# Optimization experiments

Hardware: AMD Instinct MI355X
Metric: run time of the kernel (lower is better)

## Reference

```python
import jax, jax.numpy as jnp
import numpy as np
import math

B, D, NH, NS, NT = 16, 256, 512, 8, 32
NV = NS * NT          # 256 prediction variables
L, H, A = 4, 8, 64    # attention layers, heads, head dim
HA = H * A            # 512
M = 512               # mlp_dim
R = 128               # resolution
EPS = 1e-5


def setup_inputs() -> dict:
    key = jax.random.key(0)
    ks = jax.random.split(key, 32)
    s = 0.02
    inp = {
        'hist_encoded': jax.random.normal(ks[0], (B, NH, D), jnp.float32),
        'hist_true_u': jax.random.uniform(ks[1], (B, NH), jnp.float32),
        'pred_encoded': jax.random.normal(ks[2], (B, NV, D), jnp.float32),
        'pred_true_u': jax.random.uniform(ks[3], (B, NV), jnp.float32),
        # dimension shifting layer
        'ds_w': jax.random.normal(ks[4], (D, HA), jnp.float32) * s,
        'ds_b': jnp.zeros((HA,), jnp.float32),
        # per-layer, per-head key/value creators: Linear(D+1 -> A)
        'key_w': jax.random.normal(ks[5], (L, H, D + 1, A), jnp.float32) * s,
        'key_b': jnp.zeros((L, H, A), jnp.float32),
        'val_w': jax.random.normal(ks[6], (L, H, D + 1, A), jnp.float32) * s,
        'val_b': jnp.zeros((L, H, A), jnp.float32),
        # layer norms
        'ln1_g': jnp.ones((L, HA), jnp.float32),
        'ln1_b': jnp.zeros((L, HA), jnp.float32),
        'ln2_g': jnp.ones((L, HA), jnp.float32),
        'ln2_b': jnp.zeros((L, HA), jnp.float32),
        # feed-forward (mlp_layers=2): HA->M, M->M, M->HA
        'ff_w1': jax.random.normal(ks[7], (L, HA, M), jnp.float32) * s,
        'ff_b1': jnp.zeros((L, M), jnp.float32),
        'ff_w2': jax.random.normal(ks[8], (L, M, M), jnp.float32) * s,
        'ff_b2': jnp.zeros((L, M), jnp.float32),
        'ff_w3': jax.random.normal(ks[9], (L, M, HA), jnp.float32) * s,
        'ff_b3': jnp.zeros((L, HA), jnp.float32),
        # dist extractor
        'de_w': jax.random.normal(ks[10], (HA, R), jnp.float32) * s,
        'de_b': jnp.zeros((R,), jnp.float32),
        'num_series': NS,
        'num_timesteps': NT,
    }
    return inp


def _ln(x, g, b):
    m = x.mean(-1, keepdims=True)
    v = ((x - m) ** 2).mean(-1, keepdims=True)
    return g * (x - m) / jnp.sqrt(v + EPS) + b


def _forward(hist_encoded, hist_true_u, pred_encoded, pred_true_u,
             ds_w, ds_b, key_w, key_b, val_w, val_b,
             ln1_g, ln1_b, ln2_g, ln2_b,
             ff_w1, ff_b1, ff_w2, ff_b2, ff_w3, ff_b3,
             de_w, de_b):
    Bm, NVm, Dm = pred_encoded.shape
    NHm = hist_encoded.shape[1]
    Lm, Hm, _, Am = key_w.shape
    W = NHm + NVm
    # identity permutation in the source loss() -> no-op
    att = pred_encoded @ ds_w + ds_b  # [B, NV, HA]
    # key/value inputs: [hist||u ; pred||u] -> [B, W, D+1]
    ki = jnp.concatenate([
        jnp.concatenate([hist_encoded, hist_true_u[:, :, None]], axis=2),
        jnp.concatenate([pred_encoded, pred_true_u[:, :, None]], axis=2)], axis=1)
    keys = jnp.einsum('bwd,lhda->lbhwa', ki, key_w) + key_b[:, None, :, None, :]
    vals = jnp.einsum('bwd,lhda->lbhwa', ki, val_w) + val_b[:, None, :, None, :]
    # flipped-triangular mask: position w is masked iff w >= NH + v
    mask = jnp.arange(W)[None, :] >= (NHm + jnp.arange(NVm)[:, None])  # [NV, W]
    scale = Am ** (-0.5)
    for l in range(Lm):
        avh = att.reshape(Bm, NVm, Hm, Am)
        prod = jnp.einsum('bvhi,bhwi->bhvw', avh, keys[l])  # [B,H,NV,W]
        prod = jnp.where(mask, -jnp.inf, prod) * scale
        w = jax.nn.softmax(prod, axis=-1)
        a = jnp.einsum('bhvw,bhwj->bvhj', w, vals[l]).reshape(Bm, NVm, Hm * Am)
        att = _ln(att + a, ln1_g[l], ln1_b[l])
        ff = jnp.maximum(att @ ff_w1[l] + ff_b1[l], 0.0)
        ff = jnp.maximum(ff @ ff_w2[l] + ff_b2[l], 0.0)
        ff = ff @ ff_w3[l] + ff_b3[l]
        att = _ln(att + ff, ln2_g[l], ln2_b[l])
    res = de_w.shape[-1]
    target = jnp.clip(jnp.floor(pred_true_u[:, 1:] * res).astype(jnp.int32), 0, res - 1)
    logits = (att @ de_w + de_b)[:, 1:, :]
    lp = math.log(res) + jax.nn.log_softmax(logits, axis=2)
    lp = jnp.take_along_axis(lp, target[:, :, None], axis=2)[:, :, 0]
    return -lp.sum(axis=1)  # [B]


def reference(hist_encoded, hist_true_u, pred_encoded, pred_true_u,
              ds_w, ds_b, key_w, key_b, val_w, val_b,
              ln1_g, ln1_b, ln2_g, ln2_b,
              ff_w1, ff_b1, ff_w2, ff_b2, ff_w3, ff_b3,
              de_w, de_b, num_series, num_timesteps):
    assert pred_encoded.shape[1] == num_series * num_timesteps
    return _forward(hist_encoded, hist_true_u, pred_encoded, pred_true_u,
                    ds_w, ds_b, key_w, key_b, val_w, val_b,
                    ln1_g, ln1_b, ln2_g, ln2_b,
                    ff_w1, ff_b1, ff_w2, ff_b2, ff_w3, ff_b3,
                    de_w, de_b)
```

## Files before the change

### kernel.cpp

```cpp
#include <hip/hip_runtime.h>

constexpr int kB = 16, kD = 256, kNH = 512, kNV = 256, kW = 768;
constexpr int kL = 4, kH = 8, kA = 64, kHA = 512, kM = 512, kR = 128;
constexpr int kKP = 288;
constexpr int kRows = kB * kNV;

typedef __bf16 bf16x8 __attribute__((ext_vector_type(8)));
typedef __bf16 bf16x4 __attribute__((ext_vector_type(4)));
typedef __bf16 bf16x2 __attribute__((ext_vector_type(2)));
typedef float f32x4 __attribute__((ext_vector_type(4)));

__device__ inline void load_lds16(const __bf16* g, __bf16* l) {
  __builtin_amdgcn_global_load_lds(
      (const __attribute__((address_space(1))) void*)g,
      (__attribute__((address_space(3))) void*)l, 16, 0, 0);
}

constexpr int kPrepBlocks = 10769;

__global__ void prep_kernel(const float* __restrict__ hist,
                            const float* __restrict__ hist_u,
                            const float* __restrict__ pred,
                            const float* __restrict__ pred_u,
                            const float* __restrict__ kw,
                            const float* __restrict__ vw,
                            const float* __restrict__ w1,
                            const float* __restrict__ w2,
                            const float* __restrict__ w3,
                            const float* __restrict__ ds_w,
                            const float* __restrict__ de_w,
                            const float* __restrict__ key_b,
                            const float* __restrict__ val_b,
                            __bf16* __restrict__ ki,
                            __bf16* __restrict__ kvwt,
                            __bf16* __restrict__ ffwt,
                            __bf16* __restrict__ ds_wt,
                            __bf16* __restrict__ de_wt,
                            float* __restrict__ kvb,
                            float* __restrict__ outz) {
  __shared__ float ld[2080];
  const int bid = blockIdx.x;
  const int t = threadIdx.x;
  if (bid < 6912) {
    int i = bid * 512 + t * 2;
    __bf16 v2[2];
#pragma unroll
    for (int e = 0; e < 2; ++e) {
      int ii = i + e;
      int d = ii % kKP;
      int bw = ii / kKP;
      int w = bw % kW;
      int b = bw / kW;
      float v = 0.f;
      if (d < 257) {
        if (w < kNH)
          v = (d < kD) ? hist[((size_t)b * kNH + w) * kD + d]
                       : hist_u[b * kNH + w];
        else {
          int p = w - kNH;
          v = (d < kD) ? pred[((size_t)b * kNV + p) * kD + d]
                       : pred_u[b * kNV + p];
        }
      }
      v2[e] = (__bf16)v;
    }
    *(bf16x2*)&ki[i] = bf16x2{v2[0], v2[1]};
  } else if (bid < 7488) {
    int bb = bid - 6912;
    bool isv = bb >= 288;
    int rem = isv ? bb - 288 : bb;
    int pair = rem / 9;
    int dt = rem - pair * 9;
    int d0 = dt * 32;
    const float* src = (isv ? vw : kw) + (size_t)pair * 257 * 64;
    int a = t & 63, dg = t >> 6;
#pragma unroll
    for (int ii = 0; ii < 8; ++ii) {
      int d = d0 + dg * 8 + ii;
      ld[(dg * 8 + ii) * 65 + a] = (d < 257) ? src[(size_t)d * 64 + a] : 0.f;
    }
    __syncthreads();
    int r = t >> 2, seg = t & 3;
    bf16x8 v;
#pragma unroll
    for (int j = 0; j < 8; ++j) v[j] = (__bf16)ld[(seg * 8 + j) * 65 + r];
    *(bf16x8*)&kvwt[((size_t)(isv ? 2048 : 0) + pair * 64 + r) * 288 + d0 +
                    seg * 8] = v;
  } else if (bid < 10560) {
    int cc = bid - 7488;
    int mat = cc >> 8;
    int tile = cc & 255;
    int n0 = (tile & 15) * 32, k0 = (tile >> 4) * 32;
    int l = mat / 3, which = mat - l * 3;
    const float* src = (which == 0 ? w1 : which == 1 ? w2 : w3) +
                       (size_t)l * 262144;
    int col = t & 31, kr = t >> 5;
#pragma unroll
    for (int p = 0; p < 4; ++p)
      ld[(kr + p * 8) * 33 + col] = src[(size_t)(k0 + kr + p * 8) * 512 + n0 + col];
    __syncthreads();
    int nr = t >> 3, seg = t & 7;
    bf16x4 v;
#pragma unroll
    for (int j = 0; j < 4; ++j) v[j] = (__bf16)ld[(seg * 4 + j) * 33 + nr];
    *(bf16x4*)&ffwt[(size_t)mat * 262144 + (n0 + nr) * 512 + k0 + seg * 4] = v;
  } else if (bid < 10688) {
    int cc = bid - 10560;
    int n0 = (cc & 15) * 32, k0 = (cc >> 4) * 32;
    int col = t & 31, kr = t >> 5;
#pragma unroll
    for (int p = 0; p < 4; ++p)
      ld[(kr + p * 8) * 33 + col] = ds_w[(size_t)(k0 + kr + p * 8) * 512 + n0 + col];
    __syncthreads();
    int nr = t >> 3, seg = t & 7;
    bf16x4 v;
#pragma unroll
    for (int j = 0; j < 4; ++j) v[j] = (__bf16)ld[(seg * 4 + j) * 33 + nr];
    *(bf16x4*)&ds_wt[(n0 + nr) * 256 + k0 + seg * 4] = v;
  } else if (bid < 10752) {
    int cc = bid - 10688;
    int n0 = (cc & 3) * 32, k0 = (cc >> 2) * 32;
    int col = t & 31, kr = t >> 5;
#pragma unroll
    for (int p = 0; p < 4; ++p)
      ld[(kr + p * 8) * 33 + col] = de_w[(size_t)(k0 + kr + p * 8) * 128 + n0 + col];
    __syncthreads();
    int nr = t >> 3, seg = t & 7;
    bf16x4 v;
#pragma unroll
    for (int j = 0; j < 4; ++j) v[j] = (__bf16)ld[(seg * 4 + j) * 33 + nr];
    *(bf16x4*)&de_wt[(n0 + nr) * 512 + k0 + seg * 4] = v;
  } else {
    int j = (bid - 10752) * 256 + t;
    if (j < 4096) {
      bool isv = j >= 2048;
      int cc = isv ? j - 2048 : j;
      int l = cc >> 9, rest = cc & 511;
      kvb[j] = isv ? val_b[l * 512 + rest] : key_b[l * 512 + rest];
    } else if (j < 4112) {
      outz[j - 4096] = 0.f;
    }
  }
}

template <int BN, int OMODE, bool RELU, bool KIMAP, bool BIASROW, int DEPTH>
__device__ __forceinline__ void gemm_core(
    int bxv, int byv, const __bf16* __restrict__ A,
    const __bf16* __restrict__ Bt, const float* __restrict__ bias,
    void* __restrict__ Cout, __bf16* __restrict__ Cout2, int K, int lda,
    int ldc, __bf16* Sm) {
  constexpr int JN = BN / 32;
  constexpr int BROWS = BN / 4;
  constexpr int SSTEP = (128 + BN) * 32;
  constexpr int LPS = (BN == 128) ? 4 : 3;
  constexpr int AH = DEPTH - 1;
  const int t = threadIdx.x;
  const int wid = t >> 6;
  const int lane = t & 63;
  const int bm = byv * 128;
  const int bn = bxv * BN;
  const int wm = (wid >> 1) * 64;
  const int wn = (wid & 1) * (BN / 2);
  const int sr = lane >> 2, sc = lane & 3;
  const int skey = (sr >> 1) & 3;
  const int abase = KIMAP ? ((bm >> 8) * 768 + 512 + (bm & 255)) : bm;
  const __bf16* Ag = A + (size_t)(abase + wid * 32 + sr) * lda + (sc ^ skey) * 8;
  const __bf16* Bg = Bt + (size_t)(bn + wid * BROWS + sr) * K + (sc ^ skey) * 8;

  auto stage = [&](int k0, __bf16* buf) {
    __bf16* As = buf;
    __bf16* Bs = buf + 4096;
    load_lds16(Ag + k0, As + (wid * 32) * 32);
    load_lds16(Ag + (size_t)16 * lda + k0, As + (wid * 32 + 16) * 32);
    load_lds16(Bg + k0, Bs + (wid * BROWS) * 32);
    if (BN == 128)
      load_lds16(Bg + (size_t)16 * K + k0, Bs + (wid * BROWS + 16) * 32);
  };

  f32x4 acc[4][JN] = {};
  const int q = lane >> 4, mr = lane & 15;
  const int rkey = (mr >> 1) & 3;
  const int nst = K >> 5;
  __bf16* b0 = Sm;
  __bf16* b1 = Sm + SSTEP;
  __bf16* b2 = Sm + 2 * SSTEP;
  __bf16* b3 = (DEPTH == 4) ? Sm + 3 * SSTEP : nullptr;
  stage(0, b0);
  stage(32, b1);
  if constexpr (DEPTH == 4) stage(64, b2);
  asm volatile("s_waitcnt vmcnt(%0)" ::"n"((AH - 1) * LPS) : "memory");
  __builtin_amdgcn_s_barrier();
  for (int k = 0; k < nst; ++k) {
    if (k + AH < nst) {
      if constexpr (DEPTH == 4) stage((k + AH) << 5, b3);
      else stage((k + AH) << 5, b2);
    }
    bf16x8 af[4], bfr[JN];
#pragma unroll
    for (int i = 0; i < 4; ++i)
      af[i] = *(const bf16x8*)(b0 + (wm + i * 16 + mr) * 32 + (q ^ rkey) * 8);
#pragma unroll
    for (int j = 0; j < JN; ++j)
      bfr[j] =
          *(const bf16x8*)(b0 + 4096 + (wn + j * 16 + mr) * 32 + (q ^ rkey) * 8);
#pragma unroll
    for (int i = 0; i < 4; ++i)
#pragma unroll
      for (int j = 0; j < JN; ++j)
        acc[i][j] = __builtin_amdgcn_mfma_f32_16x16x32_bf16(af[i], bfr[j],
                                                            acc[i][j], 0, 0, 0);
    if (k + AH + 1 <= nst)
      asm volatile("s_waitcnt vmcnt(%0)" ::"n"((AH - 1) * LPS) : "memory");
    else if (DEPTH == 4 && k + AH == nst + 1)
      asm volatile("s_waitcnt vmcnt(%0)" ::"n"(LPS) : "memory");
    else
      asm volatile("s_waitcnt vmcnt(0)" ::: "memory");
    __builtin_amdgcn_s_barrier();
    if constexpr (DEPTH == 4) {
      __bf16* tp = b0; b0 = b1; b1 = b2; b2 = b3; b3 = tp;
    } else {
      __bf16* tp = b0; b0 = b1; b1 = b2; b2 = tp;
    }
  }
  if (OMODE == 1) {
    constexpr int PS = BN + 8;
    __bf16* Cs = Sm;
#pragma unroll
    for (int j = 0; j < JN; ++j) {
      float bscol = BIASROW ? 0.f : bias[bn + wn + j * 16 + mr];
#pragma unroll
      for (int i = 0; i < 4; ++i) {
#pragma unroll
        for (int r = 0; r < 4; ++r) {
          float v = acc[i][j][r] +
                    (BIASROW ? bias[bm + wm + i * 16 + q * 4 + r] : bscol);
          if (RELU) v = fmaxf(v, 0.f);
          Cs[(wm + i * 16 + q * 4 + r) * PS + wn + j * 16 + mr] = (__bf16)v;
        }
      }
    }
    __syncthreads();
    constexpr int lpr = BN / 8;
    constexpr int rpi = 512 / BN;
    const int rl = lane / lpr, cl = (lane % lpr) * 8;
#pragma unroll
    for (int it = 0; it < BN / 16; ++it) {
      int row = wid * 32 + it * rpi + rl;
      bf16x8 v = *(const bf16x8*)&Cs[row * PS + cl];
      *(bf16x8*)((__bf16*)Cout + (size_t)(bm + row) * ldc + bn + cl) = v;
    }
  } else {
    constexpr int PSF = BN + 4;
    float* Csf = (float*)Sm;
#pragma unroll
    for (int j = 0; j < JN; ++j) {
      float bscol = bias[bn + wn + j * 16 + mr];
#pragma unroll
      for (int i = 0; i < 4; ++i) {
#pragma unroll
        for (int r = 0; r < 4; ++r) {
          float v = acc[i][j][r] + bscol;
          if (RELU) v = fmaxf(v, 0.f);
          Csf[(wm + i * 16 + q * 4 + r) * PSF + wn + j * 16 + mr] = v;
        }
      }
    }
    __syncthreads();
    const int rl = lane >> 4, cl = (lane & 15) * 4;
#pragma unroll
    for (int it = 0; it < 8; ++it) {
      int row = wid * 32 + it * 4 + rl;
      f32x4 v = *(const f32x4*)&Csf[row * PSF + cl];
      size_t gidx = (size_t)(bm + row) * ldc + bn + cl;
      *(f32x4*)((float*)Cout + gidx) = v;
      bf16x4 vb = {(__bf16)v[0], (__bf16)v[1], (__bf16)v[2], (__bf16)v[3]};
      *(bf16x4*)(Cout2 + gidx) = vb;
    }
  }
}

__global__ __launch_bounds__(256) void gemm3_kernel(
    const __bf16* __restrict__ ki, const __bf16* __restrict__ ds_wt,
    const float* __restrict__ ds_b, float* __restrict__ att,
    __bf16* __restrict__ att_bf, const __bf16* __restrict__ kv_wt,
    const float* __restrict__ kvb, __bf16* __restrict__ kvs_k,
    __bf16* __restrict__ vT) {
  __shared__ __bf16 smem[32768];
  int bid = blockIdx.x;
  if (bid < 256) {
    gemm_core<64, 2, false, true, false, 3>(bid & 7, bid >> 3, ki, ds_wt, ds_b,
                                            att, att_bf, 256, kKP, 512, smem);
  } else if (bid < 1792) {
    int b2 = bid - 256;
    gemm_core<128, 1, false, false, false, 4>(b2 & 15, b2 >> 4, ki, kv_wt, kvb,
                                              kvs_k, nullptr, kKP, kKP, 2048,
                                              smem);
  } else {
    int b3 = bid - 1792;
    gemm_core<128, 1, false, false, true, 4>(b3 % 96, b3 / 96,
                                             kv_wt + (size_t)2048 * kKP, ki,
                                             kvb + 2048, vT, nullptr, kKP, kKP,
                                             12288, smem);
  }
}

template <bool RELU>
__global__ __launch_bounds__(256) void gemm_ff_kernel(
    const __bf16* __restrict__ A, const __bf16* __restrict__ Bt,
    const float* __restrict__ bias, __bf16* __restrict__ Cout) {
  __shared__ __bf16 smem[24576];
  gemm_core<64, 1, RELU, false, false, 4>(blockIdx.x, blockIdx.y, A, Bt, bias,
                                          Cout, nullptr, 512, 512, 512, smem);
}

__global__ __launch_bounds__(256) void attn_mfma_kernel(
    const __bf16* __restrict__ attbf, const __bf16* __restrict__ kvs_k,
    const __bf16* __restrict__ vT, __bf16* __restrict__ outbf, int l) {
  const int id = blockIdx.x;
  const int kk = id >> 3;
  const int b = ((kk >> 5) << 3) | (id & 7);
  const int qt = kk & 3;
  const int h = (kk >> 2) & 7;
  __shared__ __bf16 Ks[2][64 * 72];
  __shared__ __bf16 Vt[2][64 * 72];
  __shared__ __bf16 Ps[64 * 72];
  const int t = threadIdx.x;
  const int w = t >> 6, lane = t & 63;
  const int quad = lane >> 4, mr = lane & 15;
  bf16x8 aq[2];
  {
    const __bf16* qp = attbf + ((size_t)(b * kNV + qt * 64 + w * 16 + mr) * kHA +
                                h * kA + quad * 8);
    aq[0] = *(const bf16x8*)qp;
    aq[1] = *(const bf16x8*)(qp + 32);
  }
  f32x4 o[4] = {};
  float m_ = -1e30f, l_ = 0.f;
  const int cmax = kNH + qt * 64;
  const int nt = (cmax >> 6) + 1;
  const int pr = t >> 2, pc = t & 3;
  const __bf16* kbase = kvs_k + ((size_t)(b * kW + pr) * 2048 + l * 512 + h * kA);
  const __bf16* vbase = vT + (size_t)(l * 512 + h * kA + pr) * 12288 + b * kW;
  bf16x8 kc0, kc1, vc0, vc1;
  auto loadt = [&](int tt) {
    const __bf16* kp = kbase + (size_t)(tt << 6) * 2048;
    const __bf16* vp = vbase + (tt << 6);
    kc0 = *(const bf16x8*)(kp + pc * 8);
    kc1 = *(const bf16x8*)(kp + pc * 8 + 32);
    vc0 = *(const bf16x8*)(vp + pc * 16);
    vc1 = *(const bf16x8*)(vp + pc * 16 + 8);
  };
  auto writet = [&](int buf) {
    *(bf16x8*)&Ks[buf][pr * 72 + pc * 8] = kc0;
    *(bf16x8*)&Ks[buf][pr * 72 + pc * 8 + 32] = kc1;
    *(bf16x8*)&Vt[buf][pr * 72 + pc * 16] = vc0;
    *(bf16x8*)&Vt[buf][pr * 72 + pc * 16 + 8] = vc1;
  };
  loadt(0);
  writet(0);
  if (nt > 1) loadt(1);
  __syncthreads();
  for (int tt = 0; tt < nt; ++tt) {
    const int cur = tt & 1;
    f32x4 s[4];
#pragma unroll
    for (int j = 0; j < 4; ++j) {
      bf16x8 ak0 = *(const bf16x8*)&Ks[cur][(j * 16 + mr) * 72 + quad * 8];
      bf16x8 ak1 = *(const bf16x8*)&Ks[cur][(j * 16 + mr) * 72 + quad * 8 + 32];
      f32x4 z = {};
      z = __builtin_amdgcn_mfma_f32_16x16x32_bf16(ak0, aq[0], z, 0, 0, 0);
      z = __builtin_amdgcn_mfma_f32_16x16x32_bf16(ak1, aq[1], z, 0, 0, 0);
      s[j] = z;
    }
    const int lim = cmax - (tt << 6);
    float sv[16], mx = -1e30f;
#pragma unroll
    for (int j = 0; j < 4; ++j)
#pragma unroll
      for (int r = 0; r < 4; ++r) {
        int p = j * 16 + quad * 4 + r;
        float x = (p < lim + mr) ? s[j][r] * 0.125f : -1e30f;
        sv[j * 4 + r] = x;
        mx = fmaxf(mx, x);
      }
    mx = fmaxf(mx, __shfl_xor(mx, 16));
    mx = fmaxf(mx, __shfl_xor(mx, 32));
    float mnew = fmaxf(m_, mx);
    float corr = __expf(m_ - mnew);
    float rs = 0.f;
#pragma unroll
    for (int i = 0; i < 16; ++i) {
      sv[i] = __expf(sv[i] - mnew);
      rs += sv[i];
    }
    rs += __shfl_xor(rs, 16);
    rs += __shfl_xor(rs, 32);
    l_ = l_ * corr + rs;
    m_ = mnew;
#pragma unroll
    for (int j = 0; j < 4; ++j) {
      bf16x4 pk = {(__bf16)sv[j * 4 + 0], (__bf16)sv[j * 4 + 1],
                   (__bf16)sv[j * 4 + 2], (__bf16)sv[j * 4 + 3]};
      *(bf16x4*)&Ps[(w * 16 + mr) * 72 + j * 16 + quad * 4] = pk;
    }
#pragma unroll
    for (int r = 0; r < 4; ++r) {
      float cr = __shfl(corr, quad * 4 + r);
#pragma unroll
      for (int j = 0; j < 4; ++j) o[j][r] *= cr;
    }
    bf16x8 ap0 = *(const bf16x8*)&Ps[(w * 16 + mr) * 72 + quad * 8];
    bf16x8 ap1 = *(const bf16x8*)&Ps[(w * 16 + mr) * 72 + quad * 8 + 32];
#pragma unroll
    for (int j = 0; j < 4; ++j) {
      bf16x8 b0 = *(const bf16x8*)&Vt[cur][(j * 16 + mr) * 72 + quad * 8];
      bf16x8 b1 = *(const bf16x8*)&Vt[cur][(j * 16 + mr) * 72 + quad * 8 + 32];
      o[j] = __builtin_amdgcn_mfma_f32_16x16x32_bf16(ap0, b0, o[j], 0, 0, 0);
      o[j] = __builtin_amdgcn_mfma_f32_16x16x32_bf16(ap1, b1, o[j], 0, 0, 0);
    }
    if (tt + 1 < nt) {
      writet(cur ^ 1);
      if (tt + 2 < nt) loadt(tt + 2);
      __syncthreads();
    }
  }
  float invl = 1.f / l_;
#pragma unroll
  for (int r = 0; r < 4; ++r) {
    float ir = __shfl(invl, quad * 4 + r);
    int row = b * kNV + qt * 64 + w * 16 + quad * 4 + r;
#pragma unroll
    for (int j = 0; j < 4; ++j)
      outbf[(size_t)row * kHA + h * kA + j * 16 + mr] = (__bf16)(o[j][r] * ir);
  }
}

__global__ __launch_bounds__(256) void add_ln_kernel(
    float* __restrict__ att, const __bf16* __restrict__ addbf,
    const float* __restrict__ g, const float* __restrict__ be,
    __bf16* __restrict__ attbf) {
  const int w = threadIdx.x >> 6, lane = threadIdx.x & 63;
  const int row = blockIdx.x * 4 + w;
  const int c0 = lane * 8;
  const size_t base = (size_t)row * kHA + c0;
  float4 a0 = *(const float4*)(att + base);
  float4 a1 = *(const float4*)(att + base + 4);
  bf16x8 dv = *(const bf16x8*)(addbf + base);
  float x[8] = {a0.x + (float)dv[0], a0.y + (float)dv[1], a0.z + (float)dv[2],
                a0.w + (float)dv[3], a1.x + (float)dv[4], a1.y + (float)dv[5],
                a1.z + (float)dv[6], a1.w + (float)dv[7]};
  float s = 0.f, q = 0.f;
#pragma unroll
  for (int j = 0; j < 8; ++j) { s += x[j]; q += x[j] * x[j]; }
#pragma unroll
  for (int o = 1; o < 64; o <<= 1) {
    s += __shfl_xor(s, o);
    q += __shfl_xor(q, o);
  }
  const float mean = s * (1.f / kHA);
  const float inv = rsqrtf(q * (1.f / kHA) - mean * mean + 1e-5f);
  float4 g0 = *(const float4*)(g + c0);
  float4 g1 = *(const float4*)(g + c0 + 4);
  float4 e0 = *(const float4*)(be + c0);
  float4 e1 = *(const float4*)(be + c0 + 4);
  float y[8];
  y[0] = g0.x * (x[0] - mean) * inv + e0.x;
  y[1] = g0.y * (x[1] - mean) * inv + e0.y;
  y[2] = g0.z * (x[2] - mean) * inv + e0.z;
  y[3] = g0.w * (x[3] - mean) * inv + e0.w;
  y[4] = g1.x * (x[4] - mean) * inv + e1.x;
  y[5] = g1.y * (x[5] - mean) * inv + e1.y;
  y[6] = g1.z * (x[6] - mean) * inv + e1.z;
  y[7] = g1.w * (x[7] - mean) * inv + e1.w;
  *(float4*)(att + base) = (float4){y[0], y[1], y[2], y[3]};
  *(float4*)(att + base + 4) = (float4){y[4], y[5], y[6], y[7]};
  bf16x8 yb = {(__bf16)y[0], (__bf16)y[1], (__bf16)y[2], (__bf16)y[3],
               (__bf16)y[4], (__bf16)y[5], (__bf16)y[6], (__bf16)y[7]};
  *(bf16x8*)(attbf + base) = yb;
}

__global__ __launch_bounds__(256) void de_loss_kernel(
    const float* __restrict__ att, const __bf16* __restrict__ fbf,
    const float* __restrict__ g2, const float* __restrict__ b2,
    const __bf16* __restrict__ de_wt, const float* __restrict__ de_b,
    const float* __restrict__ pred_u, float* __restrict__ out) {
  __shared__ __bf16 Als[64 * 512];
  __shared__ float red[4];
  const int blk = blockIdx.x;
  const int t = threadIdx.x;
  const int w = t >> 6, lane = t & 63, quad = lane >> 4, mr = lane & 15;
  {
    const int c0 = lane * 8;
    float4 ga = *(const float4*)(g2 + c0);
    float4 gb = *(const float4*)(g2 + c0 + 4);
    float4 ba = *(const float4*)(b2 + c0);
    float4 bb = *(const float4*)(b2 + c0 + 4);
    for (int rr = 0; rr < 16; ++rr) {
      const int lrow = w * 16 + rr;
      const size_t base = (size_t)(blk * 64 + lrow) * 512 + c0;
      float4 a0 = *(const float4*)(att + base);
      float4 a1 = *(const float4*)(att + base + 4);
      bf16x8 dv = *(const bf16x8*)(fbf + base);
      float x[8] = {a0.x + (float)dv[0], a0.y + (float)dv[1],
                    a0.z + (float)dv[2], a0.w + (float)dv[3],
                    a1.x + (float)dv[4], a1.y + (float)dv[5],
                    a1.z + (float)dv[6], a1.w + (float)dv[7]};
      float s = 0.f, q = 0.f;
#pragma unroll
      for (int j = 0; j < 8; ++j) { s += x[j]; q += x[j] * x[j]; }
#pragma unroll
      for (int o = 1; o < 64; o <<= 1) {
        s += __shfl_xor(s, o);
        q += __shfl_xor(q, o);
      }
      const float mean = s * (1.f / kHA);
      const float inv = rsqrtf(q * (1.f / kHA) - mean * mean + 1e-5f);
      bf16x8 yv = {(__bf16)(ga.x * (x[0] - mean) * inv + ba.x),
                   (__bf16)(ga.y * (x[1] - mean) * inv + ba.y),
                   (__bf16)(ga.z * (x[2] - mean) * inv + ba.z),
                   (__bf16)(ga.w * (x[3] - mean) * inv + ba.w),
                   (__bf16)(gb.x * (x[4] - mean) * inv + bb.x),
                   (__bf16)(gb.y * (x[5] - mean) * inv + bb.y),
                   (__bf16)(gb.z * (x[6] - mean) * inv + bb.z),
                   (__bf16)(gb.w * (x[7] - mean) * inv + bb.w)};
      *(bf16x8*)&Als[lrow * 512 + ((lane ^ (lrow & 7)) << 3)] = yv;
    }
  }
  __syncthreads();
  const int row0 = blk * 64 + w * 16;
  const int lrowA = w * 16 + mr;
  f32x4 acc[8] = {};
#pragma unroll 4
  for (int k0 = 0; k0 < 512; k0 += 32) {
    const int grp = (((k0 >> 3) + quad) ^ (lrowA & 7)) << 3;
    bf16x8 a = *(const bf16x8*)&Als[lrowA * 512 + grp];
#pragma unroll
    for (int j = 0; j < 8; ++j) {
      bf16x8 bb =
          *(const bf16x8*)(de_wt + (size_t)(j * 16 + mr) * 512 + k0 + quad * 8);
      acc[j] = __builtin_amdgcn_mfma_f32_16x16x32_bf16(a, bb, acc[j], 0, 0, 0);
    }
  }
  float dbv[8];
#pragma unroll
  for (int j = 0; j < 8; ++j) dbv[j] = de_b[j * 16 + mr];
  float lpacc = 0.f;
#pragma unroll
  for (int r = 0; r < 4; ++r) {
    int row = row0 + quad * 4 + r;
    int v = row & 255;
    float lg[8], mx = -1e30f;
#pragma unroll
    for (int j = 0; j < 8; ++j) {
      lg[j] = acc[j][r] + dbv[j];
      mx = fmaxf(mx, lg[j]);
    }
    mx = fmaxf(mx, __shfl_xor(mx, 1));
    mx = fmaxf(mx, __shfl_xor(mx, 2));
    mx = fmaxf(mx, __shfl_xor(mx, 4));
    mx = fmaxf(mx, __shfl_xor(mx, 8));
    float se = 0.f;
#pragma unroll
    for (int j = 0; j < 8; ++j) se += __expf(lg[j] - mx);
    se += __shfl_xor(se, 1);
    se += __shfl_xor(se, 2);
    se += __shfl_xor(se, 4);
    se += __shfl_xor(se, 8);
    float lse = mx + __logf(se);
    float u = pred_u[(row >> 8) * 256 + v];
    int tgt = (int)floorf(u * 128.f);
    tgt = max(0, min(127, tgt));
    float cand = (mr == (tgt & 15)) ? lg[tgt >> 4] : 0.f;
    cand += __shfl_xor(cand, 1);
    cand += __shfl_xor(cand, 2);
    cand += __shfl_xor(cand, 4);
    cand += __shfl_xor(cand, 8);
    float lp = (v >= 1) ? (4.8520302639196171f + cand - lse) : 0.f;
    lpacc += lp;
  }
  lpacc += __shfl_xor(lpacc, 16);
  lpacc += __shfl_xor(lpacc, 32);
  if (lane == 0) red[w] = lpacc;
  __syncthreads();
  if (t == 0)
    atomicAdd(&out[blk >> 2], -(red[0] + red[1] + red[2] + red[3]));
}

extern "C" void kernel_launch(void* const* d_in, const int* in_sizes, int n_in,
                              void* d_out, int out_size, void* d_ws, size_t ws_size,
                              hipStream_t stream) {
  const float* hist   = (const float*)d_in[0];
  const float* hist_u = (const float*)d_in[1];
  const float* pred   = (const float*)d_in[2];
  const float* pred_u = (const float*)d_in[3];
  const float* ds_w   = (const float*)d_in[4];
  const float* ds_b   = (const float*)d_in[5];
  const float* key_w  = (const float*)d_in[6];
  const float* key_b  = (const float*)d_in[7];
  const float* val_w  = (const float*)d_in[8];
  const float* val_b  = (const float*)d_in[9];
  const float* ln1_g  = (const float*)d_in[10];
  const float* ln1_b  = (const float*)d_in[11];
  const float* ln2_g  = (const float*)d_in[12];
  const float* ln2_b  = (const float*)d_in[13];
  const float* ff_w1  = (const float*)d_in[14];
  const float* ff_b1  = (const float*)d_in[15];
  const float* ff_w2  = (const float*)d_in[16];
  const float* ff_b2  = (const float*)d_in[17];
  const float* ff_w3  = (const float*)d_in[18];
  const float* ff_b3  = (const float*)d_in[19];
  const float* de_w   = (const float*)d_in[20];
  const float* de_b   = (const float*)d_in[21];
  float* out = (float*)d_out;

  char* ws = (char*)d_ws;
  size_t off = 0;
  auto alloc = [&](size_t bytes) { char* p = ws + off; off += bytes; return p; };
  __bf16* ki_bf  = (__bf16*)alloc((size_t)kB * kW * kKP * 2);
  __bf16* kv_wt  = (__bf16*)alloc((size_t)4096 * kKP * 2);
  __bf16* ffw_t  = (__bf16*)alloc((size_t)12 * 512 * 512 * 2);
  __bf16* ds_wt  = (__bf16*)alloc((size_t)512 * 256 * 2);
  __bf16* de_wt  = (__bf16*)alloc((size_t)128 * 512 * 2);
  float*  kvb    = (float*)alloc((size_t)4096 * 4);
  __bf16* kvs_k  = (__bf16*)alloc((size_t)kB * kW * 2048 * 2);
  __bf16* vT     = (__bf16*)alloc((size_t)2048 * 12288 * 2);
  float*  att    = (float*)alloc((size_t)kRows * kHA * 4);
  __bf16* att_bf = (__bf16*)alloc((size_t)kRows * kHA * 2);
  __bf16* tmp_bf = (__bf16*)alloc((size_t)kRows * kHA * 2);
  __bf16* ff1_bf = (__bf16*)alloc((size_t)kRows * kM * 2);
  __bf16* ff2_bf = (__bf16*)alloc((size_t)kRows * kM * 2);

  prep_kernel<<<kPrepBlocks, 256, 0, stream>>>(
      hist, hist_u, pred, pred_u, key_w, val_w, ff_w1, ff_w2, ff_w3, ds_w, de_w,
      key_b, val_b, ki_bf, kv_wt, ffw_t, ds_wt, de_wt, kvb, out);

  gemm3_kernel<<<3328, 256, 0, stream>>>(ki_bf, ds_wt, ds_b, att, att_bf, kv_wt,
                                         kvb, kvs_k, vT);

  for (int l = 0; l < kL; ++l) {
    attn_mfma_kernel<<<512, 256, 0, stream>>>(att_bf, kvs_k, vT, tmp_bf, l);
    add_ln_kernel<<<kRows / 4, 256, 0, stream>>>(att, tmp_bf, ln1_g + l * kHA,
                                                 ln1_b + l * kHA, att_bf);
    gemm_ff_kernel<true><<<dim3(kM / 64, kRows / 128), 256, 0, stream>>>(
        att_bf, ffw_t + (size_t)(l * 3) * 262144, ff_b1 + l * kM, ff1_bf);
    gemm_ff_kernel<true><<<dim3(kM / 64, kRows / 128), 256, 0, stream>>>(
        ff1_bf, ffw_t + (size_t)(l * 3 + 1) * 262144, ff_b2 + l * kM, ff2_bf);
    gemm_ff_kernel<false><<<dim3(kHA / 64, kRows / 128), 256, 0, stream>>>(
        ff2_bf, ffw_t + (size_t)(l * 3 + 2) * 262144, ff_b3 + l * kHA, tmp_bf);
    if (l < kL - 1)
      add_ln_kernel<<<kRows / 4, 256, 0, stream>>>(att, tmp_bf,
                                                   ln2_g + l * kHA,
                                                   ln2_b + l * kHA, att_bf);
  }
  de_loss_kernel<<<64, 256, 0, stream>>>(att, tmp_bf, ln2_g + 3 * kHA,
                                         ln2_b + 3 * kHA, de_wt, de_b, pred_u,
                                         out);
}
```

Before: 412.2 us.

## Fuse LayerNorms into first and last feed-forward GEMM kernels

```diff
diff --git a/kernel.cpp b/kernel.cpp
--- a/kernel.cpp
+++ b/kernel.cpp
@@ -311,6 +311,254 @@
   __shared__ __bf16 smem[24576];
   gemm_core<64, 1, RELU, false, false, 4>(blockIdx.x, blockIdx.y, A, Bt, bias,
                                           Cout, nullptr, 512, 512, 512, smem);
+}
+
+__global__ __launch_bounds__(512) void ff1f_kernel(
+    float* __restrict__ att, const __bf16* __restrict__ atmp,
+    const float* __restrict__ g1, const float* __restrict__ b1,
+    const __bf16* __restrict__ Wt, const float* __restrict__ fb1,
+    __bf16* __restrict__ f1) {
+  __shared__ __bf16 Als[64 * 512];
+  __shared__ __bf16 Bsm[3 * 4096];
+  __shared__ __bf16 Cs[64 * 136];
+  const int blk = blockIdx.x;
+  const int tid = threadIdx.x;
+  const int w = tid >> 6, lane = tid & 63;
+  const int quad = lane >> 4, mr = lane & 15;
+  const int rowg = w >> 1, colw = w & 1;
+  {
+    const int c0 = lane * 8;
+    float4 ga = *(const float4*)(g1 + c0);
+    float4 gb = *(const float4*)(g1 + c0 + 4);
+    float4 ba = *(const float4*)(b1 + c0);
+    float4 bb = *(const float4*)(b1 + c0 + 4);
+#pragma unroll
+    for (int it = 0; it < 8; ++it) {
+      const int lrow = w * 8 + it;
+      const size_t base = (size_t)(blk * 64 + lrow) * 512 + c0;
+      float4 a0 = *(const float4*)(att + base);
+      float4 a1 = *(const float4*)(att + base + 4);
+      bf16x8 dv = *(const bf16x8*)(atmp + base);
+      float x[8] = {a0.x + (float)dv[0], a0.y + (float)dv[1],
+                    a0.z + (float)dv[2], a0.w + (float)dv[3],
+                    a1.x + (float)dv[4], a1.y + (float)dv[5],
+                    a1.z + (float)dv[6], a1.w + (float)dv[7]};
+      float s = 0.f, q = 0.f;
+#pragma unroll
+      for (int j = 0; j < 8; ++j) { s += x[j]; q += x[j] * x[j]; }
+#pragma unroll
+      for (int o = 1; o < 64; o <<= 1) {
+        s += __shfl_xor(s, o);
+        q += __shfl_xor(q, o);
+      }
+      const float mean = s * (1.f / kHA);
+      const float inv = rsqrtf(q * (1.f / kHA) - mean * mean + 1e-5f);
+      float y[8];
+      y[0] = ga.x * (x[0] - mean) * inv + ba.x;
+      y[1] = ga.y * (x[1] - mean) * inv + ba.y;
+      y[2] = ga.z * (x[2] - mean) * inv + ba.z;
+      y[3] = ga.w * (x[3] - mean) * inv + ba.w;
+      y[4] = gb.x * (x[4] - mean) * inv + bb.x;
+      y[5] = gb.y * (x[5] - mean) * inv + bb.y;
+      y[6] = gb.z * (x[6] - mean) * inv + bb.z;
+      y[7] = gb.w * (x[7] - mean) * inv + bb.w;
+      *(float4*)(att + base) = (float4){y[0], y[1], y[2], y[3]};
+      *(float4*)(att + base + 4) = (float4){y[4], y[5], y[6], y[7]};
+      bf16x8 yv = {(__bf16)y[0], (__bf16)y[1], (__bf16)y[2], (__bf16)y[3],
+                   (__bf16)y[4], (__bf16)y[5], (__bf16)y[6], (__bf16)y[7]};
+      *(bf16x8*)&Als[lrow * 512 + ((lane ^ (lrow & 7)) << 3)] = yv;
+    }
+  }
+  __syncthreads();
+  const int sr = lane >> 2, sc = lane & 3;
+  const int skey = (sr >> 1) & 3;
+  auto stageB = [&](int s, __bf16* buf) {
+    const __bf16* src = Wt + (size_t)((s >> 4) * 128 + w * 16 + sr) * 512 +
+                        ((s & 15) << 5) + ((sc ^ skey) << 3);
+    load_lds16(src, buf + w * 512);
+  };
+  __bf16* p0 = Bsm;
+  __bf16* p1 = Bsm + 4096;
+  __bf16* p2 = Bsm + 8192;
+  stageB(0, p0);
+  stageB(1, p1);
+  asm volatile("s_waitcnt vmcnt(1)" ::: "memory");
+  __builtin_amdgcn_s_barrier();
+  const int arow = rowg * 16 + mr;
+  const int rk = (mr >> 1) & 3;
+#pragma unroll
+  for (int chunk = 0; chunk < 4; ++chunk) {
+    f32x4 acc[4] = {};
+    for (int kk = 0; kk < 16; ++kk) {
+      const int s = chunk * 16 + kk;
+      if (s + 2 < 64) stageB(s + 2, p2);
+      bf16x8 af = *(const bf16x8*)&Als[arow * 512 +
+                                       (((kk * 4 + quad) ^ (arow & 7)) << 3)];
+      bf16x8 bfr[4];
+#pragma unroll
+      for (int j = 0; j < 4; ++j)
+        bfr[j] = *(const bf16x8*)&p0[(colw * 64 + j * 16 + mr) * 32 +
+                                     ((quad ^ rk) << 3)];
+#pragma unroll
+      for (int j = 0; j < 4; ++j)
+        acc[j] = __builtin_amdgcn_mfma_f32_16x16x32_bf16(af, bfr[j], acc[j], 0,
+                                                         0, 0);
+      if (s < 61)
+        asm volatile("s_waitcnt vmcnt(1)" ::: "memory");
+      else
+        asm volatile("s_waitcnt vmcnt(0)" ::: "memory");
+      __builtin_amdgcn_s_barrier();
+      __bf16* tp = p0; p0 = p1; p1 = p2; p2 = tp;
+    }
+#pragma unroll
+    for (int j = 0; j < 4; ++j) {
+      float bc = fb1[chunk * 128 + colw * 64 + j * 16 + mr];
+#pragma unroll
+      for (int r = 0; r < 4; ++r) {
+        float v = fmaxf(acc[j][r] + bc, 0.f);
+        Cs[(rowg * 16 + quad * 4 + r) * 136 + colw * 64 + j * 16 + mr] =
+            (__bf16)v;
+      }
+    }
+    asm volatile("s_waitcnt lgkmcnt(0)" ::: "memory");
+    __builtin_amdgcn_s_barrier();
+    __builtin_amdgcn_sched_barrier(0);
+#pragma unroll
+    for (int it = 0; it < 2; ++it) {
+      int row = (tid >> 4) + it * 32;
+      int seg = tid & 15;
+      bf16x8 v = *(const bf16x8*)&Cs[row * 136 + seg * 8];
+      *(bf16x8*)&f1[(size_t)(blk * 64 + row) * 512 + chunk * 128 + seg * 8] = v;
+    }
+    __builtin_amdgcn_s_barrier();
+  }
+}
+
+__global__ __launch_bounds__(512) void ff3f_kernel(
+    const __bf16* __restrict__ f2, const __bf16* __restrict__ Wt,
+    const float* __restrict__ fb3, float* __restrict__ att,
+    const float* __restrict__ g2, const float* __restrict__ b2,
+    __bf16* __restrict__ attbf) {
+  __shared__ __bf16 Als[64 * 512];
+  __shared__ __bf16 Bsm[3 * 4096];
+  __shared__ float red2[8][32];
+  const int blk = blockIdx.x;
+  const int tid = threadIdx.x;
+  const int w = tid >> 6, lane = tid & 63;
+  const int quad = lane >> 4, mr = lane & 15;
+  const int rowg = w >> 1, colw = w & 1;
+#pragma unroll
+  for (int i = 0; i < 8; ++i) {
+    const int row = i * 8 + w;
+    load_lds16(f2 + (size_t)(blk * 64 + row) * 512 + ((lane ^ (row & 7)) << 3),
+               Als + row * 512);
+  }
+  const int sr = lane >> 2, sc = lane & 3;
+  const int skey = (sr >> 1) & 3;
+  auto stageB = [&](int s, __bf16* buf) {
+    const __bf16* src = Wt + (size_t)((s >> 4) * 128 + w * 16 + sr) * 512 +
+                        ((s & 15) << 5) + ((sc ^ skey) << 3);
+    load_lds16(src, buf + w * 512);
+  };
+  __bf16* p0 = Bsm;
+  __bf16* p1 = Bsm + 4096;
+  __bf16* p2 = Bsm + 8192;
+  stageB(0, p0);
+  stageB(1, p1);
+  asm volatile("s_waitcnt vmcnt(1)" ::: "memory");
+  __builtin_amdgcn_s_barrier();
+  const int arow = rowg * 16 + mr;
+  const int rk = (mr >> 1) & 3;
+  f32x4 accs[4][4] = {};
+#pragma unroll
+  for (int chunk = 0; chunk < 4; ++chunk) {
+    for (int kk = 0; kk < 16; ++kk) {
+      const int s = chunk * 16 + kk;
+      if (s + 2 < 64) stageB(s + 2, p2);
+      bf16x8 af = *(const bf16x8*)&Als[arow * 512 +
+                                       (((kk * 4 + quad) ^ (arow & 7)) << 3)];
+      bf16x8 bfr[4];
+#pragma unroll
+      for (int j = 0; j < 4; ++j)
+        bfr[j] = *(const bf16x8*)&p0[(colw * 64 + j * 16 + mr) * 32 +
+                                     ((quad ^ rk) << 3)];
+#pragma unroll
+      for (int j = 0; j < 4; ++j)
+        accs[chunk][j] = __builtin_amdgcn_mfma_f32_16x16x32_bf16(
+            af, bfr[j], accs[chunk][j], 0, 0, 0);
+      if (s < 61)
+        asm volatile("s_waitcnt vmcnt(1)" ::: "memory");
+      else
+        asm volatile("s_waitcnt vmcnt(0)" ::: "memory");
+      __builtin_amdgcn_s_barrier();
+      __bf16* tp = p0; p0 = p1; p1 = p2; p2 = tp;
+    }
+  }
+  float ps[4] = {}, pq[4] = {};
+#pragma unroll
+  for (int chunk = 0; chunk < 4; ++chunk) {
+#pragma unroll
+    for (int j = 0; j < 4; ++j) {
+      const int col = chunk * 128 + colw * 64 + j * 16 + mr;
+      const float bv = fb3[col];
+#pragma unroll
+      for (int r = 0; r < 4; ++r) {
+        const int R = blk * 64 + rowg * 16 + quad * 4 + r;
+        float x = accs[chunk][j][r] + bv + att[(size_t)R * 512 + col];
+        accs[chunk][j][r] = x;
+        ps[r] += x;
+        pq[r] += x * x;
+      }
+    }
+  }
+#pragma unroll
+  for (int r = 0; r < 4; ++r)
+#pragma unroll
+    for (int o = 1; o < 16; o <<= 1) {
+      ps[r] += __shfl_xor(ps[r], o);
+      pq[r] += __shfl_xor(pq[r], o);
+    }
+  if (mr == 0) {
+#pragma unroll
+    for (int r = 0; r < 4; ++r) {
+      red2[w][quad * 4 + r] = ps[r];
+      red2[w][16 + quad * 4 + r] = pq[r];
+    }
+  }
+  __syncthreads();
+  float mean_[4], inv_[4];
+#pragma unroll
+  for (int r = 0; r < 4; ++r) {
+    const int qr = quad * 4 + r;
+    float S = red2[rowg * 2][qr] + red2[rowg * 2 + 1][qr];
+    float Q = red2[rowg * 2][16 + qr] + red2[rowg * 2 + 1][16 + qr];
+    mean_[r] = S * (1.f / kHA);
+    inv_[r] = rsqrtf(Q * (1.f / kHA) - mean_[r] * mean_[r] + 1e-5f);
+  }
+  __syncthreads();
+#pragma unroll
+  for (int chunk = 0; chunk < 4; ++chunk) {
+#pragma unroll
+    for (int j = 0; j < 4; ++j) {
+      const int col = chunk * 128 + colw * 64 + j * 16 + mr;
+      const float gv = g2[col], bvv = b2[col];
+#pragma unroll
+      for (int r = 0; r < 4; ++r) {
+        const int lrow = rowg * 16 + quad * 4 + r;
+        const float z = gv * (accs[chunk][j][r] - mean_[r]) * inv_[r] + bvv;
+        att[(size_t)(blk * 64 + lrow) * 512 + col] = z;
+        Als[lrow * 512 + col] = (__bf16)z;
+      }
+    }
+  }
+  __syncthreads();
+#pragma unroll
+  for (int i = 0; i < 8; ++i) {
+    const int gidx = i * 512 + tid;
+    const int row = gidx >> 6, grp = gidx & 63;
+    bf16x8 v = *(const bf16x8*)&Als[row * 512 + grp * 8];
+    *(bf16x8*)&attbf[(size_t)(blk * 64 + row) * 512 + grp * 8] = v;
+  }
 }
 
 __global__ __launch_bounds__(256) void attn_mfma_kernel(
@@ -435,105 +683,19 @@
   }
 }
 
-__global__ __launch_bounds__(256) void add_ln_kernel(
-    float* __restrict__ att, const __bf16* __restrict__ addbf,
-    const float* __restrict__ g, const float* __restrict__ be,
-    __bf16* __restrict__ attbf) {
-  const int w = threadIdx.x >> 6, lane = threadIdx.x & 63;
-  const int row = blockIdx.x * 4 + w;
-  const int c0 = lane * 8;
-  const size_t base = (size_t)row * kHA + c0;
-  float4 a0 = *(const float4*)(att + base);
-  float4 a1 = *(const float4*)(att + base + 4);
-  bf16x8 dv = *(const bf16x8*)(addbf + base);
-  float x[8] = {a0.x + (float)dv[0], a0.y + (float)dv[1], a0.z + (float)dv[2],
-                a0.w + (float)dv[3], a1.x + (float)dv[4], a1.y + (float)dv[5],
-                a1.z + (float)dv[6], a1.w + (float)dv[7]};
-  float s = 0.f, q = 0.f;
-#pragma unroll
-  for (int j = 0; j < 8; ++j) { s += x[j]; q += x[j] * x[j]; }
-#pragma unroll
-  for (int o = 1; o < 64; o <<= 1) {
-    s += __shfl_xor(s, o);
-    q += __shfl_xor(q, o);
-  }
-  const float mean = s * (1.f / kHA);
-  const float inv = rsqrtf(q * (1.f / kHA) - mean * mean + 1e-5f);
-  float4 g0 = *(const float4*)(g + c0);
-  float4 g1 = *(const float4*)(g + c0 + 4);
-  float4 e0 = *(const float4*)(be + c0);
-  float4 e1 = *(const float4*)(be + c0 + 4);
-  float y[8];
-  y[0] = g0.x * (x[0] - mean) * inv + e0.x;
-  y[1] = g0.y * (x[1] - mean) * inv + e0.y;
-  y[2] = g0.z * (x[2] - mean) * inv + e0.z;
-  y[3] = g0.w * (x[3] - mean) * inv + e0.w;
-  y[4] = g1.x * (x[4] - mean) * inv + e1.x;
-  y[5] = g1.y * (x[5] - mean) * inv + e1.y;
-  y[6] = g1.z * (x[6] - mean) * inv + e1.z;
-  y[7] = g1.w * (x[7] - mean) * inv + e1.w;
-  *(float4*)(att + base) = (float4){y[0], y[1], y[2], y[3]};
-  *(float4*)(att + base + 4) = (float4){y[4], y[5], y[6], y[7]};
-  bf16x8 yb = {(__bf16)y[0], (__bf16)y[1], (__bf16)y[2], (__bf16)y[3],
-               (__bf16)y[4], (__bf16)y[5], (__bf16)y[6], (__bf16)y[7]};
-  *(bf16x8*)(attbf + base) = yb;
-}
-
 __global__ __launch_bounds__(256) void de_loss_kernel(
-    const float* __restrict__ att, const __bf16* __restrict__ fbf,
-    const float* __restrict__ g2, const float* __restrict__ b2,
-    const __bf16* __restrict__ de_wt, const float* __restrict__ de_b,
-    const float* __restrict__ pred_u, float* __restrict__ out) {
-  __shared__ __bf16 Als[64 * 512];
-  __shared__ float red[4];
+    const __bf16* __restrict__ attbf, const __bf16* __restrict__ de_wt,
+    const float* __restrict__ de_b, const float* __restrict__ pred_u,
+    float* __restrict__ out) {
   const int blk = blockIdx.x;
   const int t = threadIdx.x;
   const int w = t >> 6, lane = t & 63, quad = lane >> 4, mr = lane & 15;
-  {
-    const int c0 = lane * 8;
-    float4 ga = *(const float4*)(g2 + c0);
-    float4 gb = *(const float4*)(g2 + c0 + 4);
-    float4 ba = *(const float4*)(b2 + c0);
-    float4 bb = *(const float4*)(b2 + c0 + 4);
-    for (int rr = 0; rr < 16; ++rr) {
-      const int lrow = w * 16 + rr;
-      const size_t base = (size_t)(blk * 64 + lrow) * 512 + c0;
-      float4 a0 = *(const float4*)(att + base);
-      float4 a1 = *(const float4*)(att + base + 4);
-      bf16x8 dv = *(const bf16x8*)(fbf + base);
-      float x[8] = {a0.x + (float)dv[0], a0.y + (float)dv[1],
-                    a0.z + (float)dv[2], a0.w + (float)dv[3],
-                    a1.x + (float)dv[4], a1.y + (float)dv[5],
-                    a1.z + (float)dv[6], a1.w + (float)dv[7]};
-      float s = 0.f, q = 0.f;
-#pragma unroll
-      for (int j = 0; j < 8; ++j) { s += x[j]; q += x[j] * x[j]; }
-#pragma unroll
-      for (int o = 1; o < 64; o <<= 1) {
-        s += __shfl_xor(s, o);
-        q += __shfl_xor(q, o);
-      }
-      const float mean = s * (1.f / kHA);
-      const float inv = rsqrtf(q * (1.f / kHA) - mean * mean + 1e-5f);
-      bf16x8 yv = {(__bf16)(ga.x * (x[0] - mean) * inv + ba.x),
-                   (__bf16)(ga.y * (x[1] - mean) * inv + ba.y),
-                   (__bf16)(ga.z * (x[2] - mean) * inv + ba.z),
-                   (__bf16)(ga.w * (x[3] - mean) * inv + ba.w),
-                   (__bf16)(gb.x * (x[4] - mean) * inv + bb.x),
-                   (__bf16)(gb.y * (x[5] - mean) * inv + bb.y),
-                   (__bf16)(gb.z * (x[6] - mean) * inv + bb.z),
-                   (__bf16)(gb.w * (x[7] - mean) * inv + bb.w)};
-      *(bf16x8*)&Als[lrow * 512 + ((lane ^ (lrow & 7)) << 3)] = yv;
-    }
-  }
-  __syncthreads();
   const int row0 = blk * 64 + w * 16;
-  const int lrowA = w * 16 + mr;
   f32x4 acc[8] = {};
+  const __bf16* Ap = attbf + (size_t)(row0 + mr) * kHA + quad * 8;
 #pragma unroll 4
   for (int k0 = 0; k0 < 512; k0 += 32) {
-    const int grp = (((k0 >> 3) + quad) ^ (lrowA & 7)) << 3;
-    bf16x8 a = *(const bf16x8*)&Als[lrowA * 512 + grp];
+    bf16x8 a = *(const bf16x8*)(Ap + k0);
 #pragma unroll
     for (int j = 0; j < 8; ++j) {
       bf16x8 bb =
@@ -580,6 +742,7 @@
   }
   lpacc += __shfl_xor(lpacc, 16);
   lpacc += __shfl_xor(lpacc, 32);
+  __shared__ float red[4];
   if (lane == 0) red[w] = lpacc;
   __syncthreads();
   if (t == 0)
@@ -639,20 +802,15 @@
 
   for (int l = 0; l < kL; ++l) {
     attn_mfma_kernel<<<512, 256, 0, stream>>>(att_bf, kvs_k, vT, tmp_bf, l);
-    add_ln_kernel<<<kRows / 4, 256, 0, stream>>>(att, tmp_bf, ln1_g + l * kHA,
-                                                 ln1_b + l * kHA, att_bf);
-    gemm_ff_kernel<true><<<dim3(kM / 64, kRows / 128), 256, 0, stream>>>(
-        att_bf, ffw_t + (size_t)(l * 3) * 262144, ff_b1 + l * kM, ff1_bf);
+    ff1f_kernel<<<64, 512, 0, stream>>>(att, tmp_bf, ln1_g + l * kHA,
+                                        ln1_b + l * kHA,
+                                        ffw_t + (size_t)(l * 3) * 262144,
+                                        ff_b1 + l * kM, ff1_bf);
     gemm_ff_kernel<true><<<dim3(kM / 64, kRows / 128), 256, 0, stream>>>(
         ff1_bf, ffw_t + (size_t)(l * 3 + 1) * 262144, ff_b2 + l * kM, ff2_bf);
-    gemm_ff_kernel<false><<<dim3(kHA / 64, kRows / 128), 256, 0, stream>>>(
-        ff2_bf, ffw_t + (size_t)(l * 3 + 2) * 262144, ff_b3 + l * kHA, tmp_bf);
-    if (l < kL - 1)
-      add_ln_kernel<<<kRows / 4, 256, 0, stream>>>(att, tmp_bf,
-                                                   ln2_g + l * kHA,
-                                                   ln2_b + l * kHA, att_bf);
-  }
-  de_loss_kernel<<<64, 256, 0, stream>>>(att, tmp_bf, ln2_g + 3 * kHA,
-                                         ln2_b + 3 * kHA, de_wt, de_b, pred_u,
-                                         out);
-}
+    ff3f_kernel<<<64, 512, 0, stream>>>(
+        ff2_bf, ffw_t + (size_t)(l * 3 + 2) * 262144, ff_b3 + l * kHA, att,
+        ln2_g + l * kHA, ln2_b + l * kHA, att_bf);
+  }
+  de_loss_kernel<<<64, 256, 0, stream>>>(att_bf, de_wt, de_b, pred_u, out);
+}
```

After: 501.2 us. 21.6% more time.
